# Performance work log

Hardware: AMD Instinct MI355X
Metric: run time of the kernel (lower is better)

Reference implementation:

```python
import jax, jax.numpy as jnp
import numpy as np


def setup_inputs() -> dict:
    key = jax.random.key(0)
    k1, k2 = jax.random.split(key)
    n, c, h, w = 8, 2048, 64, 64
    out_c = 512
    fea = jax.random.normal(k1, (n, c, h, w), dtype=jnp.float32)
    # Conv2d weight [out, in, kh=1, kw=9]; kaiming-ish scale
    W = jax.random.normal(k2, (out_c, c, 1, 9), dtype=jnp.float32) * 0.02
    b = jnp.zeros((out_c,), dtype=jnp.float32)
    return {"fea": fea, "W": W, "b": b}


def reference(fea, W, b):
    # Original module (stride=1 path): for each width column i, take the
    # [n,c,h,1] slice, run Conv2d(kernel=(1,9), pad=(0,4)) + ReLU, concat on w.
    # For a width-1 input, only the CENTER kernel tap (kw index 4) overlaps
    # real data; all other taps see zero padding. Hence each column output is
    # ReLU(W[:,:,0,4] @ column + b), and the concat over columns is exactly a
    # pointwise (1x1) conv over the full feature map with the center tap.
    Wc = W[:, :, 0, 4]  # [out_c, in_c]
    out = jnp.einsum('nchw,oc->nohw', fea, Wc) + b[None, :, None, None]
    return jax.nn.relu(out)
```

## Files before the change

kernel.cpp:

```cpp
#include <hip/hip_runtime.h>
#include <hip/hip_bf16.h>

typedef __bf16 bf16x4 __attribute__((ext_vector_type(4)));
typedef __bf16 bf16x8 __attribute__((ext_vector_type(8)));
typedef float floatx4 __attribute__((ext_vector_type(4)));

#define KDIM 2048
#define MDIM 512
#define HWDIM 4096
#define BN 64
#define BK 32
#define NITER (KDIM / BK)

__global__ void extract_w_kernel(const float* __restrict__ W, __bf16* __restrict__ Wc) {
  int e = (blockIdx.x * 256 + threadIdx.x) * 4;
  bf16x4 h;
#pragma unroll
  for (int j = 0; j < 4; ++j) h[j] = (__bf16)W[(size_t)(e + j) * 9 + 4];
  *(bf16x4*)(Wc + e) = h;
}

__global__ __launch_bounds__(512, 4) void conv1x1_kernel(
    const float* __restrict__ fea, const __bf16* __restrict__ Wc,
    const float* __restrict__ bias, float* __restrict__ out) {
  __shared__ __align__(16) __bf16 Bs[2][BN * BK];

  const int t    = threadIdx.x;
  const int wave = t >> 6;
  const int lane = t & 63;
  const int l15  = lane & 15;
  const int quad = lane >> 4;
  const int wm   = wave * 64;

  const int img = blockIdx.x >> 6;
  const int nb  = blockIdx.x & 63;

  const float* feaN = fea + (size_t)img * KDIM * HWDIM + (size_t)nb * BN;
  float*       outN = out + (size_t)img * MDIM * HWDIM + (size_t)nb * BN;

  const bool stager = (wave < 4);
  const int  hw   = lane;
  const int  g    = wave & 3;
  const int  boff = hw * BK + ((g ^ ((hw >> 1) & 3)) * 8);
  const float* bsrc = feaN + (size_t)g * 8 * HWDIM + hw;

  const __bf16* aptr = Wc + (size_t)(wm + l15) * KDIM + quad * 8;

  float bpf[2][8];
  floatx4 acc[4][4];
#pragma unroll
  for (int i = 0; i < 4; ++i)
#pragma unroll
    for (int j = 0; j < 4; ++j) acc[i][j] = (floatx4){0.f, 0.f, 0.f, 0.f};

  if (stager) {
#pragma unroll
    for (int j = 0; j < 8; ++j) bpf[0][j] = bsrc[(size_t)j * HWDIM];
#pragma unroll
    for (int j = 0; j < 8; ++j) bpf[1][j] = bsrc[(size_t)(BK + j) * HWDIM];
    bf16x8 h0;
#pragma unroll
    for (int j = 0; j < 8; ++j) h0[j] = (__bf16)bpf[0][j];
    *(bf16x8*)&Bs[0][boff] = h0;
  }
  __syncthreads();

#define KBODY(I, CUR)                                                          \
  {                                                                            \
    const int i_ = (I);                                                        \
    bf16x8 af[4];                                                              \
    const __bf16* ap = aptr + i_ * BK;                                         \
    _Pragma("unroll")                                                          \
    for (int mt = 0; mt < 4; ++mt)                                             \
      af[mt] = *(const bf16x8*)(ap + (size_t)mt * 16 * KDIM);                  \
    if (stager && i_ + 1 < NITER) {                                            \
      bf16x8 hn;                                                               \
      _Pragma("unroll")                                                        \
      for (int j = 0; j < 8; ++j) hn[j] = (__bf16)bpf[(CUR) ^ 1][j];           \
      *(bf16x8*)&Bs[(CUR) ^ 1][boff] = hn;                                     \
    }                                                                          \
    if (stager && i_ + 2 < NITER) {                                            \
      const float* p = bsrc + (size_t)(i_ + 2) * BK * HWDIM;                   \
      _Pragma("unroll")                                                        \
      for (int j = 0; j < 8; ++j) bpf[(CUR)][j] = p[(size_t)j * HWDIM];        \
    }                                                                          \
    _Pragma("unroll")                                                          \
    for (int nt = 0; nt < 4; ++nt) {                                           \
      const int n_ = nt * 16 + l15;                                            \
      const bf16x8 bfr =                                                       \
          *(const bf16x8*)&Bs[(CUR)][n_ * BK + ((quad ^ ((n_ >> 1) & 3)) * 8)];\
      _Pragma("unroll")                                                        \
      for (int mt = 0; mt < 4; ++mt)                                           \
        acc[mt][nt] = __builtin_amdgcn_mfma_f32_16x16x32_bf16(af[mt], bfr,     \
                                                              acc[mt][nt],    \
                                                              0, 0, 0);       \
    }                                                                          \
    __syncthreads();                                                           \
  }

  for (int i = 0; i < NITER; i += 2) {
    KBODY(i, 0)
    KBODY(i + 1, 1)
  }
#undef KBODY

#pragma unroll
  for (int mt = 0; mt < 4; ++mt) {
    const int o0 = wm + mt * 16 + quad * 4;
    const float4 bv = *(const float4*)(bias + o0);
    const float bvr[4] = {bv.x, bv.y, bv.z, bv.w};
#pragma unroll
    for (int r = 0; r < 4; ++r) {
      const size_t ro = (size_t)(o0 + r) * HWDIM;
#pragma unroll
      for (int nt = 0; nt < 4; ++nt) {
        float x = acc[mt][nt][r] + bvr[r];
        outN[ro + nt * 16 + l15] = x > 0.f ? x : 0.f;
      }
    }
  }
}

extern "C" void kernel_launch(void* const* d_in, const int* in_sizes, int n_in,
                              void* d_out, int out_size, void* d_ws, size_t ws_size,
                              hipStream_t stream) {
  const float* fea  = (const float*)d_in[0];
  const float* W    = (const float*)d_in[1];
  const float* bias = (const float*)d_in[2];
  float* out = (float*)d_out;
  __bf16* Wc = (__bf16*)d_ws;

  hipLaunchKernelGGL(extract_w_kernel, dim3(1024), dim3(256), 0, stream, W, Wc);
  hipLaunchKernelGGL(conv1x1_kernel, dim3(512), dim3(512), 0, stream, fea, Wc, bias, out);
}
```

Before: 484.4 us.

## Double K tile to 64 with all waves staging B, lighter barriers, coalesced weight extract

The K tile grows from 32 to 64, so all eight waves now convert and stage B into shared memory instead of only four, and the main loop runs half as many barriers. The full __syncthreads is replaced by an LDS-only waitcnt plus s_barrier, which avoids waiting on outstanding global prefetches. The XOR swizzle is updated for the wider row. The weight extraction kernel now reads W with coalesced float4 loads across more blocks and writes only the centre-tap elements, instead of doing strided scalar loads.

```diff
diff --git a/kernel.cpp b/kernel.cpp
--- a/kernel.cpp
+++ b/kernel.cpp
@@ -1,7 +1,6 @@
 #include <hip/hip_runtime.h>
 #include <hip/hip_bf16.h>
 
-typedef __bf16 bf16x4 __attribute__((ext_vector_type(4)));
 typedef __bf16 bf16x8 __attribute__((ext_vector_type(8)));
 typedef float floatx4 __attribute__((ext_vector_type(4)));
 
@@ -9,15 +8,19 @@
 #define MDIM 512
 #define HWDIM 4096
 #define BN 64
-#define BK 32
+#define BK 64
 #define NITER (KDIM / BK)
 
 __global__ void extract_w_kernel(const float* __restrict__ W, __bf16* __restrict__ Wc) {
-  int e = (blockIdx.x * 256 + threadIdx.x) * 4;
-  bf16x4 h;
+  const int idx = blockIdx.x * 256 + threadIdx.x;
+  const float4 v = ((const float4*)W)[idx];
+  const float vv[4] = {v.x, v.y, v.z, v.w};
+  const int f0 = idx * 4;
 #pragma unroll
-  for (int j = 0; j < 4; ++j) h[j] = (__bf16)W[(size_t)(e + j) * 9 + 4];
-  *(bf16x4*)(Wc + e) = h;
+  for (int j = 0; j < 4; ++j) {
+    const int f = f0 + j;
+    if (f % 9 == 4) Wc[f / 9] = (__bf16)vv[j];
+  }
 }
 
 __global__ __launch_bounds__(512, 4) void conv1x1_kernel(
@@ -38,11 +41,9 @@
   const float* feaN = fea + (size_t)img * KDIM * HWDIM + (size_t)nb * BN;
   float*       outN = out + (size_t)img * MDIM * HWDIM + (size_t)nb * BN;
 
-  const bool stager = (wave < 4);
-  const int  hw   = lane;
-  const int  g    = wave & 3;
-  const int  boff = hw * BK + ((g ^ ((hw >> 1) & 3)) * 8);
-  const float* bsrc = feaN + (size_t)g * 8 * HWDIM + hw;
+  const int hw   = lane;
+  const int boff = hw * BK + ((wave ^ (hw & 7)) * 8);
+  const float* bsrc = feaN + (size_t)wave * 8 * HWDIM + hw;
 
   const __bf16* aptr = Wc + (size_t)(wm + l15) * KDIM + quad * 8;
 
@@ -53,49 +54,58 @@
 #pragma unroll
     for (int j = 0; j < 4; ++j) acc[i][j] = (floatx4){0.f, 0.f, 0.f, 0.f};
 
-  if (stager) {
 #pragma unroll
-    for (int j = 0; j < 8; ++j) bpf[0][j] = bsrc[(size_t)j * HWDIM];
+  for (int j = 0; j < 8; ++j) bpf[0][j] = bsrc[(size_t)j * HWDIM];
 #pragma unroll
-    for (int j = 0; j < 8; ++j) bpf[1][j] = bsrc[(size_t)(BK + j) * HWDIM];
+  for (int j = 0; j < 8; ++j) bpf[1][j] = bsrc[(size_t)(BK + j) * HWDIM];
+  {
     bf16x8 h0;
 #pragma unroll
     for (int j = 0; j < 8; ++j) h0[j] = (__bf16)bpf[0][j];
     *(bf16x8*)&Bs[0][boff] = h0;
   }
-  __syncthreads();
+  asm volatile("s_waitcnt lgkmcnt(0)" ::: "memory");
+  __builtin_amdgcn_s_barrier();
+  asm volatile("" ::: "memory");
 
 #define KBODY(I, CUR)                                                          \
   {                                                                            \
     const int i_ = (I);                                                        \
-    bf16x8 af[4];                                                              \
-    const __bf16* ap = aptr + i_ * BK;                                         \
+    bf16x8 af[2][4];                                                           \
+    const __bf16* ap = aptr + (size_t)i_ * BK;                                 \
     _Pragma("unroll")                                                          \
-    for (int mt = 0; mt < 4; ++mt)                                             \
-      af[mt] = *(const bf16x8*)(ap + (size_t)mt * 16 * KDIM);                  \
-    if (stager && i_ + 1 < NITER) {                                            \
+    for (int s = 0; s < 2; ++s)                                                \
+      _Pragma("unroll")                                                        \
+      for (int mt = 0; mt < 4; ++mt)                                           \
+        af[s][mt] = *(const bf16x8*)(ap + (size_t)(mt * 16) * KDIM + s * 32);  \
+    if (i_ + 1 < NITER) {                                                      \
       bf16x8 hn;                                                               \
       _Pragma("unroll")                                                        \
       for (int j = 0; j < 8; ++j) hn[j] = (__bf16)bpf[(CUR) ^ 1][j];           \
       *(bf16x8*)&Bs[(CUR) ^ 1][boff] = hn;                                     \
     }                                                                          \
-    if (stager && i_ + 2 < NITER) {                                            \
+    if (i_ + 2 < NITER) {                                                      \
       const float* p = bsrc + (size_t)(i_ + 2) * BK * HWDIM;                   \
       _Pragma("unroll")                                                        \
       for (int j = 0; j < 8; ++j) bpf[(CUR)][j] = p[(size_t)j * HWDIM];        \
     }                                                                          \
     _Pragma("unroll")                                                          \
-    for (int nt = 0; nt < 4; ++nt) {                                           \
-      const int n_ = nt * 16 + l15;                                            \
-      const bf16x8 bfr =                                                       \
-          *(const bf16x8*)&Bs[(CUR)][n_ * BK + ((quad ^ ((n_ >> 1) & 3)) * 8)];\
+    for (int s = 0; s < 2; ++s)                                                \
       _Pragma("unroll")                                                        \
-      for (int mt = 0; mt < 4; ++mt)                                           \
-        acc[mt][nt] = __builtin_amdgcn_mfma_f32_16x16x32_bf16(af[mt], bfr,     \
-                                                              acc[mt][nt],    \
-                                                              0, 0, 0);       \
+      for (int nt = 0; nt < 4; ++nt) {                                         \
+        const int n_ = nt * 16 + l15;                                          \
+        const bf16x8 bfr = *(const bf16x8*)&Bs[(CUR)][n_ * BK +                \
+                              (((s * 4 + quad) ^ (n_ & 7)) * 8)];              \
+        _Pragma("unroll")                                                      \
+        for (int mt = 0; mt < 4; ++mt)                                         \
+          acc[mt][nt] = __builtin_amdgcn_mfma_f32_16x16x32_bf16(af[s][mt],     \
+                            bfr, acc[mt][nt], 0, 0, 0);                        \
+      }                                                                        \
+    if (i_ + 1 < NITER) {                                                      \
+      asm volatile("s_waitcnt lgkmcnt(0)" ::: "memory");                       \
+      __builtin_amdgcn_s_barrier();                                            \
+      asm volatile("" ::: "memory");                                           \
     }                                                                          \
-    __syncthreads();                                                           \
   }
 
   for (int i = 0; i < NITER; i += 2) {
@@ -130,6 +140,6 @@
   float* out = (float*)d_out;
   __bf16* Wc = (__bf16*)d_ws;
 
-  hipLaunchKernelGGL(extract_w_kernel, dim3(1024), dim3(256), 0, stream, W, Wc);
+  hipLaunchKernelGGL(extract_w_kernel, dim3(9216), dim3(256), 0, stream, W, Wc);
   hipLaunchKernelGGL(conv1x1_kernel, dim3(512), dim3(512), 0, stream, fea, Wc, bias, out);
 }
```

Result: slower. 512.2 us (+5.7%).
